# Performance work log

Hardware: AMD Instinct MI355X
Metric: run time of the kernel (lower is better)

Reference implementation:

```python
import jax, jax.numpy as jnp
import numpy as np

N_NODES = 100000
N_EDGES = 3200000
D = 128


def setup_inputs() -> dict:
    key = jax.random.key(0)
    k_feat, k_src, k_dst, k_w1, k_w2 = jax.random.split(key, 5)
    feat = jax.random.normal(k_feat, (N_NODES, D), dtype=jnp.float32)
    src = jax.random.randint(k_src, (N_EDGES,), 0, N_NODES, dtype=jnp.int32)
    dst = jax.random.randint(k_dst, (N_EDGES,), 0, N_NODES, dtype=jnp.int32)
    eps = jnp.zeros((1,), dtype=jnp.float32)
    s1 = 1.0 / np.sqrt(D)
    W1 = jax.random.normal(k_w1, (D, D), dtype=jnp.float32) * s1
    b1 = jnp.zeros((D,), dtype=jnp.float32)
    W2 = jax.random.normal(k_w2, (D, D), dtype=jnp.float32) * s1
    b2 = jnp.zeros((D,), dtype=jnp.float32)
    return {"feat": feat, "src": src, "dst": dst, "eps": eps,
            "W1": W1, "b1": b1, "W2": W2, "b2": b2}


def reference(feat, src, dst, eps, W1, b1, W2, b2):
    # message passing: copy source features along edges, sum-reduce at dst
    # neigh[v] = sum_{(u,v) in E} feat[u]
    msgs = feat[src]                                  # [E, D] gather
    neigh = jax.ops.segment_sum(msgs, dst, num_segments=feat.shape[0])  # [N, D]
    # GIN update: (1 + eps) * h_v + aggregated neighbors, then MLP
    h = (1.0 + eps[0]) * feat + neigh                 # [N, D]
    h = jax.nn.relu(h @ W1 + b1)                      # [N, D]
    out = h @ W2 + b2                                 # [N, D]
    return out
```

## Files before the change

kernel.cpp:

```cpp
#include <hip/hip_runtime.h>
#include <stdint.h>

#define N_NODES 100000
#define N_EDGES 3200000
#define DIM 128
#define NPAD 100032
#define NBINS 391
#define BCAP 10240
#define EPB 4096
#define PASSU32 3200000

typedef short short8 __attribute__((ext_vector_type(8)));
typedef float f32x4 __attribute__((ext_vector_type(4)));
typedef float f32x2 __attribute__((ext_vector_type(2)));

__device__ __forceinline__ short f2bf(float x) {
    uint32_t u = __builtin_bit_cast(uint32_t, x);
    u += 0x7fffu + ((u >> 16) & 1u);
    return (short)(u >> 16);
}
__device__ __forceinline__ float bflo(uint32_t p) {
    return __builtin_bit_cast(float, p << 16);
}
__device__ __forceinline__ float bfhi(uint32_t p) {
    return __builtin_bit_cast(float, p & 0xffff0000u);
}
__device__ __forceinline__ uint32_t pack2(float x, float y) {
    return (uint32_t)(uint16_t)f2bf(x) | ((uint32_t)(uint16_t)f2bf(y) << 16);
}
__device__ __forceinline__ f32x2 up2(uint32_t p) {
    return (f32x2){ bflo(p), bfhi(p) };
}

__global__ __launch_bounds__(256) void prep_kernel(const float* __restrict__ feat,
                                                   uint32_t* __restrict__ featp,
                                                   const float* __restrict__ w1,
                                                   const float* __restrict__ w2,
                                                   short* __restrict__ w1t,
                                                   short* __restrict__ w2t,
                                                   int* __restrict__ bincnt) {
    int b = blockIdx.x, t = threadIdx.x;
    if (b < 12500) {
        int i = b * 256 + t;
        float4 f = ((const float4*)feat)[i];
        int node = i >> 5;
        int qi = i & 31;
        int p = qi >> 4;
        int ld = qi & 15;
        uint32_t* o = &featp[p * PASSU32 + node * 32 + ld * 2];
        o[0] = pack2(f.x, f.y);
        o[1] = pack2(f.z, f.w);
    } else if (b < 12564) {
        int i = (b - 12500) * 256 + t;
        int k = i >> 7, n = i & 127;
        w1t[n * DIM + k] = f2bf(w1[i]);
        w2t[n * DIM + k] = f2bf(w2[i]);
    } else {
        int i = (b - 12564) * 256 + t;
        bincnt[i] = 0;
    }
}

__global__ __launch_bounds__(256) void bin_kernel(const int* __restrict__ src,
                                                  const int* __restrict__ dst,
                                                  int* __restrict__ bincnt,
                                                  uint32_t* __restrict__ binpair) {
    __shared__ int hist[512];
    __shared__ int scanv[512];
    __shared__ int scan256[256];
    __shared__ int gbase[NBINS];
    __shared__ int cursor[NBINS];
    __shared__ uint32_t sorted[EPB];
    __shared__ int saddr[EPB];
    int t = threadIdx.x;
    for (int i = t; i < 512; i += 256) hist[i] = 0;
    __syncthreads();
    int e0 = blockIdx.x * EPB;
    int nn = min(EPB, N_EDGES - e0);
    int d[16];
#pragma unroll
    for (int i = 0; i < 16; i++) {
        int idx = i * 256 + t;
        d[i] = (idx < nn) ? dst[e0 + idx] : -1;
        if (d[i] >= 0) atomicAdd(&hist[d[i] >> 8], 1);
    }
    __syncthreads();
    int h0 = hist[2 * t], h1 = hist[2 * t + 1];
    scan256[t] = h0 + h1;
    __syncthreads();
    for (int dd = 1; dd < 256; dd <<= 1) {
        int v = (t >= dd) ? scan256[t - dd] : 0;
        __syncthreads();
        scan256[t] += v;
        __syncthreads();
    }
    int pairExcl = scan256[t] - (h0 + h1);
    scanv[2 * t] = pairExcl;
    scanv[2 * t + 1] = pairExcl + h0;
    for (int b = t; b < NBINS; b += 256) {
        int h = hist[b];
        gbase[b] = h ? atomicAdd(&bincnt[b], h) : 0;
        cursor[b] = 0;
    }
    __syncthreads();
#pragma unroll
    for (int i = 0; i < 16; i++) {
        if (d[i] >= 0) {
            int b = d[i] >> 8;
            int slot = atomicAdd(&cursor[b], 1);
            int p = scanv[b] + slot;
            int g = gbase[b] + slot;
            int e = e0 + i * 256 + t;
            sorted[p] = (uint32_t)src[e] | ((uint32_t)(d[i] & 255) << 24);
            saddr[p] = (g < BCAP) ? (b * BCAP + g) : -1;
        }
    }
    __syncthreads();
    for (int i = t; i < nn; i += 256) {
        int a = saddr[i];
        if (a >= 0) binpair[a] = sorted[i];
    }
}

__global__ __launch_bounds__(1024) void csr_kernel(const int* __restrict__ bincnt,
                                                   const uint32_t* __restrict__ binpair,
                                                   int* __restrict__ rowptr,
                                                   int* __restrict__ csr) {
    __shared__ int hist[256];
    __shared__ int cursor[256];
    __shared__ int sc[256];
    __shared__ int red[256];
    __shared__ int binbase_s;
    __shared__ int sorted_s[BCAP];
    int b = blockIdx.x;
    int t = threadIdx.x;
    if (t < 256) {
        int partial = 0;
        for (int j = t; j < b; j += 256) partial += min(bincnt[j], BCAP);
        red[t] = partial;
        hist[t] = 0;
    }
    __syncthreads();
    for (int dd = 128; dd > 0; dd >>= 1) {
        if (t < dd) red[t] += red[t + dd];
        __syncthreads();
    }
    if (t == 0) binbase_s = red[0];
    __syncthreads();
    int binbase = binbase_s;
    int cntb = min(bincnt[b], BCAP);
    const uint32_t* pairs = binpair + (size_t)b * BCAP;
    for (int i = t; i < cntb; i += 1024)
        atomicAdd(&hist[pairs[i] >> 24], 1);
    __syncthreads();
    int val = 0;
    if (t < 256) { val = hist[t]; sc[t] = val; }
    __syncthreads();
    for (int dd = 1; dd < 256; dd <<= 1) {
        int addv = (t < 256 && t >= dd) ? sc[t - dd] : 0;
        __syncthreads();
        if (t < 256) sc[t] += addv;
        __syncthreads();
    }
    if (t < 256) {
        int excl = sc[t] - val;
        rowptr[(b << 8) + t] = binbase + excl;
        cursor[t] = excl;
    }
    __syncthreads();
    for (int i = t; i < cntb; i += 1024) {
        uint32_t p = pairs[i];
        int s2 = atomicAdd(&cursor[p >> 24], 1);
        sorted_s[s2] = (int)(p & 0x00FFFFFFu);
    }
    __syncthreads();
    for (int i = t; i < cntb; i += 1024)
        csr[binbase + i] = sorted_s[i];
}

#define LDQ(qv, sl) do { int _i = __shfl(u, (sl)); \
    qv = *(const uint4*)&featp[_i * 32 + col8 * 4]; } while (0)

#define ACC8(q) do { \
    A01 += up2((q).x); A23 += up2((q).y); A45 += up2((q).z); A67 += up2((q).w); } while (0)

__global__ __launch_bounds__(256) void gather_kernel(const uint32_t* __restrict__ featp,
                                                     const int* __restrict__ rowptr,
                                                     const int* __restrict__ csr,
                                                     const float* __restrict__ eps,
                                                     uint32_t* __restrict__ hbf,
                                                     int poff) {
    int wid = blockIdx.x * 4 + (threadIdx.x >> 6);
    int lane = threadIdx.x & 63;
    int eighth = lane >> 3;
    int col8 = lane & 7;
    if (wid >= N_NODES) {
        if (wid < NPAD && lane < 32) hbf[wid * 64 + poff + lane] = 0;
        return;
    }
    float e1 = 1.0f + eps[0];
    uint4 sf = *(const uint4*)&featp[wid * 32 + col8 * 4];
    f32x2 A01 = (f32x2){0.f, 0.f}, A23 = (f32x2){0.f, 0.f};
    f32x2 A45 = (f32x2){0.f, 0.f}, A67 = (f32x2){0.f, 0.f};
    int start = rowptr[wid], end = rowptr[wid + 1];
    for (int base = start; base < end; base += 64) {
        int m = min(64, end - base);
        int u = (lane < m) ? csr[base + lane] : 0;
        int j = 0;
        for (; j + 32 <= m; j += 32) {
            uint4 q0, q1, q2, q3;
            LDQ(q0, j + eighth);
            LDQ(q1, j + 8 + eighth);
            LDQ(q2, j + 16 + eighth);
            LDQ(q3, j + 24 + eighth);
            ACC8(q0); ACC8(q1); ACC8(q2); ACC8(q3);
        }
        int r = m - j;
        if (r > 0) {
            int mm = m - 1;
            if (r > 24) {
                uint4 q0, q1, q2, q3;
                int p3 = j + 24 + eighth;
                LDQ(q0, j + eighth); LDQ(q1, j + 8 + eighth);
                LDQ(q2, j + 16 + eighth); LDQ(q3, min(p3, mm));
                ACC8(q0); ACC8(q1); ACC8(q2);
                if (p3 < m) ACC8(q3);
            } else if (r > 16) {
                uint4 q0, q1, q2;
                int p2 = j + 16 + eighth;
                LDQ(q0, j + eighth); LDQ(q1, j + 8 + eighth);
                LDQ(q2, min(p2, mm));
                ACC8(q0); ACC8(q1);
                if (p2 < m) ACC8(q2);
            } else if (r > 8) {
                uint4 q0, q1;
                int p1 = j + 8 + eighth;
                LDQ(q0, j + eighth); LDQ(q1, min(p1, mm));
                ACC8(q0);
                if (p1 < m) ACC8(q1);
            } else {
                uint4 q0;
                int p0 = j + eighth;
                LDQ(q0, min(p0, mm));
                if (p0 < m) ACC8(q0);
            }
        }
    }
    float a0 = A01.x, a1 = A01.y, a2 = A23.x, a3 = A23.y;
    float a4 = A45.x, a5 = A45.y, a6 = A67.x, a7 = A67.y;
    a0 += __shfl_xor(a0, 8);  a1 += __shfl_xor(a1, 8);
    a2 += __shfl_xor(a2, 8);  a3 += __shfl_xor(a3, 8);
    a4 += __shfl_xor(a4, 8);  a5 += __shfl_xor(a5, 8);
    a6 += __shfl_xor(a6, 8);  a7 += __shfl_xor(a7, 8);
    a0 += __shfl_xor(a0, 16); a1 += __shfl_xor(a1, 16);
    a2 += __shfl_xor(a2, 16); a3 += __shfl_xor(a3, 16);
    a4 += __shfl_xor(a4, 16); a5 += __shfl_xor(a5, 16);
    a6 += __shfl_xor(a6, 16); a7 += __shfl_xor(a7, 16);
    a0 += __shfl_xor(a0, 32); a1 += __shfl_xor(a1, 32);
    a2 += __shfl_xor(a2, 32); a3 += __shfl_xor(a3, 32);
    a4 += __shfl_xor(a4, 32); a5 += __shfl_xor(a5, 32);
    a6 += __shfl_xor(a6, 32); a7 += __shfl_xor(a7, 32);
    if (eighth == 0) {
        a0 += e1 * bflo(sf.x); a1 += e1 * bfhi(sf.x);
        a2 += e1 * bflo(sf.y); a3 += e1 * bfhi(sf.y);
        a4 += e1 * bflo(sf.z); a5 += e1 * bfhi(sf.z);
        a6 += e1 * bflo(sf.w); a7 += e1 * bfhi(sf.w);
        uint4 w;
        w.x = pack2(a0, a1); w.y = pack2(a2, a3);
        w.z = pack2(a4, a5); w.w = pack2(a6, a7);
        *(uint4*)&hbf[wid * 64 + poff + col8 * 4] = w;
    }
}

__global__ __launch_bounds__(256) void mlp_kernel(const short* __restrict__ hbf,
                                                  const short* __restrict__ w1t,
                                                  const short* __restrict__ w2t,
                                                  const float* __restrict__ b1,
                                                  const float* __restrict__ b2,
                                                  float* __restrict__ out) {
    __shared__ __align__(16) short h1s[4][16 * 136];
    const int wave = threadIdx.x >> 6;
    const int lane = threadIdx.x & 63;
    const int l15 = lane & 15;
    const int quad = lane >> 4;

    float b1v[8], b2v[8];
#pragma unroll
    for (int n = 0; n < 8; n++) {
        b1v[n] = b1[n * 16 + l15];
        b2v[n] = b2[n * 16 + l15];
    }

    const int ntiles = NPAD / 64;
    for (int tile = blockIdx.x; tile < ntiles; tile += gridDim.x) {
        int row0 = tile * 64 + wave * 16;
        f32x4 acc[8];
#pragma unroll
        for (int n = 0; n < 8; n++) acc[n] = (f32x4){0.f, 0.f, 0.f, 0.f};
#pragma unroll
        for (int kb = 0; kb < DIM; kb += 32) {
            short8 a = *(const short8*)&hbf[(row0 + l15) * DIM + kb + quad * 8];
#pragma unroll
            for (int n = 0; n < 8; n++) {
                short8 b = *(const short8*)&w1t[(n * 16 + l15) * DIM + kb + quad * 8];
                acc[n] = __builtin_amdgcn_mfma_f32_16x16x32_bf16(a, b, acc[n], 0, 0, 0);
            }
        }
#pragma unroll
        for (int n = 0; n < 8; n++) {
#pragma unroll
            for (int r = 0; r < 4; r++) {
                float v = acc[n][r] + b1v[n];
                v = v > 0.f ? v : 0.f;
                h1s[wave][(quad * 4 + r) * 136 + n * 16 + l15] = f2bf(v);
            }
        }
        __syncthreads();
        f32x4 acc2[8];
#pragma unroll
        for (int n = 0; n < 8; n++) acc2[n] = (f32x4){0.f, 0.f, 0.f, 0.f};
#pragma unroll
        for (int kb = 0; kb < DIM; kb += 32) {
            short8 a2 = *(const short8*)&h1s[wave][l15 * 136 + kb + quad * 8];
#pragma unroll
            for (int n = 0; n < 8; n++) {
                short8 b = *(const short8*)&w2t[(n * 16 + l15) * DIM + kb + quad * 8];
                acc2[n] = __builtin_amdgcn_mfma_f32_16x16x32_bf16(a2, b, acc2[n], 0, 0, 0);
            }
        }
#pragma unroll
        for (int n = 0; n < 8; n++) {
#pragma unroll
            for (int r = 0; r < 4; r++) {
                int row = row0 + quad * 4 + r;
                if (row < N_NODES)
                    out[row * DIM + n * 16 + l15] = acc2[n][r] + b2v[n];
            }
        }
        __syncthreads();
    }
}

extern "C" void kernel_launch(void* const* d_in, const int* in_sizes, int n_in,
                              void* d_out, int out_size, void* d_ws, size_t ws_size,
                              hipStream_t stream) {
    const float* feat = (const float*)d_in[0];
    const int* src    = (const int*)d_in[1];
    const int* dst    = (const int*)d_in[2];
    const float* eps  = (const float*)d_in[3];
    const float* W1   = (const float*)d_in[4];
    const float* b1   = (const float*)d_in[5];
    const float* W2   = (const float*)d_in[6];
    const float* b2   = (const float*)d_in[7];
    float* out = (float*)d_out;

    char* ws = (char*)d_ws;
    int*      bincnt  = (int*)ws;
    int*      rowptr  = (int*)(ws + 2048);
    int*      csr     = (int*)(ws + 403456);
    uint32_t* binpair = (uint32_t*)(ws + 13203456);
    uint32_t* featp   = (uint32_t*)(ws + 29218816);
    uint32_t* hbf     = (uint32_t*)(ws + 54818816);
    short*    w1t     = (short*)(ws + 80427008);
    short*    w2t     = (short*)(ws + 80459776);

    prep_kernel<<<12566, 256, 0, stream>>>(feat, featp, W1, W2, w1t, w2t, bincnt);
    bin_kernel<<<(N_EDGES + EPB - 1) / EPB, 256, 0, stream>>>(src, dst, bincnt, binpair);
    csr_kernel<<<NBINS, 1024, 0, stream>>>(bincnt, binpair, rowptr, csr);
    gather_kernel<<<NPAD / 4, 256, 0, stream>>>(featp, rowptr, csr, eps, hbf, 0);
    gather_kernel<<<NPAD / 4, 256, 0, stream>>>(featp + PASSU32, rowptr, csr, eps, hbf, 32);
    mlp_kernel<<<1563, 256, 0, stream>>>((const short*)hbf, w1t, w2t, b1, b2, out);
}
```

Before: 359.8 us.

## Stage MLP weights in LDS with persistent 512-thread blocks

The MLP kernel now copies both bf16 weight matrices into padded shared memory once per block and runs a persistent grid of 256 blocks of 8 waves. Each wave loops over 16-row groups independently. This removes the repeated global/L2 weight loads per tile and the block-wide barriers inside the loop, since each wave owns its h1 scratch. The trade-offs are more LDS per block (about 107KB), which limits occupancy, and fewer blocks overall, which can leave some CUs less busy.

```diff
diff --git a/kernel.cpp b/kernel.cpp
--- a/kernel.cpp
+++ b/kernel.cpp
@@ -9,6 +9,7 @@
 #define BCAP 10240
 #define EPB 4096
 #define PASSU32 3200000
+#define WSTR 140
 
 typedef short short8 __attribute__((ext_vector_type(8)));
 typedef float f32x4 __attribute__((ext_vector_type(4)));
@@ -272,17 +273,26 @@
     }
 }
 
-__global__ __launch_bounds__(256) void mlp_kernel(const short* __restrict__ hbf,
+__global__ __launch_bounds__(512) void mlp_kernel(const short* __restrict__ hbf,
                                                   const short* __restrict__ w1t,
                                                   const short* __restrict__ w2t,
                                                   const float* __restrict__ b1,
                                                   const float* __restrict__ b2,
                                                   float* __restrict__ out) {
-    __shared__ __align__(16) short h1s[4][16 * 136];
-    const int wave = threadIdx.x >> 6;
-    const int lane = threadIdx.x & 63;
+    __shared__ __align__(16) short w1s[128 * WSTR];
+    __shared__ __align__(16) short w2s[128 * WSTR];
+    __shared__ __align__(16) short h1s[8][16 * WSTR];
+    const int t = threadIdx.x;
+    for (int c = t; c < 2048; c += 512) {
+        int row = c >> 4, cp = c & 15;
+        *(short8*)&w1s[row * WSTR + cp * 8] = *(const short8*)&w1t[row * DIM + cp * 8];
+        *(short8*)&w2s[row * WSTR + cp * 8] = *(const short8*)&w2t[row * DIM + cp * 8];
+    }
+    const int wave = t >> 6;
+    const int lane = t & 63;
     const int l15 = lane & 15;
     const int quad = lane >> 4;
+    short* h1w = &h1s[wave][0];
 
     float b1v[8], b2v[8];
 #pragma unroll
@@ -290,10 +300,11 @@
         b1v[n] = b1[n * 16 + l15];
         b2v[n] = b2[n * 16 + l15];
     }
-
-    const int ntiles = NPAD / 64;
-    for (int tile = blockIdx.x; tile < ntiles; tile += gridDim.x) {
-        int row0 = tile * 64 + wave * 16;
+    __syncthreads();
+
+    const int ngroups = NPAD / 16;
+    for (int g = blockIdx.x * 8 + wave; g < ngroups; g += gridDim.x * 8) {
+        int row0 = g * 16;
         f32x4 acc[8];
 #pragma unroll
         for (int n = 0; n < 8; n++) acc[n] = (f32x4){0.f, 0.f, 0.f, 0.f};
@@ -302,7 +313,7 @@
             short8 a = *(const short8*)&hbf[(row0 + l15) * DIM + kb + quad * 8];
 #pragma unroll
             for (int n = 0; n < 8; n++) {
-                short8 b = *(const short8*)&w1t[(n * 16 + l15) * DIM + kb + quad * 8];
+                short8 b = *(const short8*)&w1s[(n * 16 + l15) * WSTR + kb + quad * 8];
                 acc[n] = __builtin_amdgcn_mfma_f32_16x16x32_bf16(a, b, acc[n], 0, 0, 0);
             }
         }
@@ -312,19 +323,18 @@
             for (int r = 0; r < 4; r++) {
                 float v = acc[n][r] + b1v[n];
                 v = v > 0.f ? v : 0.f;
-                h1s[wave][(quad * 4 + r) * 136 + n * 16 + l15] = f2bf(v);
-            }
-        }
-        __syncthreads();
+                h1w[(quad * 4 + r) * WSTR + n * 16 + l15] = f2bf(v);
+            }
+        }
         f32x4 acc2[8];
 #pragma unroll
         for (int n = 0; n < 8; n++) acc2[n] = (f32x4){0.f, 0.f, 0.f, 0.f};
 #pragma unroll
         for (int kb = 0; kb < DIM; kb += 32) {
-            short8 a2 = *(const short8*)&h1s[wave][l15 * 136 + kb + quad * 8];
+            short8 a2 = *(const short8*)&h1w[l15 * WSTR + kb + quad * 8];
 #pragma unroll
             for (int n = 0; n < 8; n++) {
-                short8 b = *(const short8*)&w2t[(n * 16 + l15) * DIM + kb + quad * 8];
+                short8 b = *(const short8*)&w2s[(n * 16 + l15) * WSTR + kb + quad * 8];
                 acc2[n] = __builtin_amdgcn_mfma_f32_16x16x32_bf16(a2, b, acc2[n], 0, 0, 0);
             }
         }
@@ -337,7 +347,6 @@
                     out[row * DIM + n * 16 + l15] = acc2[n][r] + b2v[n];
             }
         }
-        __syncthreads();
     }
 }
 
@@ -369,5 +378,5 @@
     csr_kernel<<<NBINS, 1024, 0, stream>>>(bincnt, binpair, rowptr, csr);
     gather_kernel<<<NPAD / 4, 256, 0, stream>>>(featp, rowptr, csr, eps, hbf, 0);
     gather_kernel<<<NPAD / 4, 256, 0, stream>>>(featp + PASSU32, rowptr, csr, eps, hbf, 32);
-    mlp_kernel<<<1563, 256, 0, stream>>>((const short*)hbf, w1t, w2t, b1, b2, out);
-}
+    mlp_kernel<<<256, 512, 0, stream>>>((const short*)hbf, w1t, w2t, b1, b2, out);
+}
```

Result: faster. 310.2 us (-13.8%).
